# Performance work log

Hardware: AMD Instinct MI355X
Metric: run time of the kernel (lower is better)

## Reference

```python
import jax, jax.numpy as jnp
import numpy as np

HID = 256
HEADS = 8
HD = HID // HEADS  # head_dim = 32


def setup_inputs() -> dict:
    key = jax.random.key(0)
    ks = jax.random.split(key, 16)
    B, N = 4, 2048
    s = 0.02
    inp = {
        'x': jax.random.normal(ks[0], (B, N, 4, HID), dtype=jnp.float32),
        'Wq': jax.random.normal(ks[1], (HID, HID), dtype=jnp.float32) * s,
        'bq': jnp.zeros((HID,), jnp.float32),
        'Wk': jax.random.normal(ks[2], (HID, HID), dtype=jnp.float32) * s,
        'bk': jnp.zeros((HID,), jnp.float32),
        'Wv': jax.random.normal(ks[3], (HID, HID), dtype=jnp.float32) * s,
        'bv': jnp.zeros((HID,), jnp.float32),
        'Wvec': jax.random.normal(ks[4], (2 * HID, HID), dtype=jnp.float32) * s,
        'Wo': jax.random.normal(ks[5], (3 * HID, HID), dtype=jnp.float32) * s,
        'bo': jnp.zeros((3 * HID,), jnp.float32),
        'Wg': jax.random.normal(ks[6], (HID, 2 * HID), dtype=jnp.float32) * s,
        'bg': jnp.zeros((HID,), jnp.float32),
        'alpha_dot': jnp.asarray(1.0, jnp.float32),
        'alpha_norm': jnp.asarray(1.0, jnp.float32),
    }
    return inp


def reference(x, Wq, bq, Wk, bk, Wv, bv, Wvec, Wo, bo, Wg, bg, alpha_dot, alpha_norm):
    B, N, _, H = x.shape
    nh, hd = HEADS, HD
    x_scalar = x[:, :, 0]          # (B,N,H)
    vec = x[:, :, 1:]              # (B,N,3,H)

    def lin(a, W, b=None):
        y = a @ W.T
        return y + b if b is not None else y

    # scalar q/k/v -> (B,heads,N,hd)
    q = lin(x_scalar, Wq, bq).reshape(B, N, nh, hd).transpose(0, 2, 1, 3)
    k = lin(x_scalar, Wk, bk).reshape(B, N, nh, hd).transpose(0, 2, 1, 3)
    v = lin(x_scalar, Wv, bv).reshape(B, N, nh, hd).transpose(0, 2, 1, 3)

    # invariant features from vector channels
    vec_proj = lin(vec, Wvec)                  # (B,N,3,2H)
    vec1, vec2 = vec_proj[..., :H], vec_proj[..., H:]
    vec_dot = jnp.sum(vec1 * vec2, axis=-2)    # (B,N,H)
    vec_norm = jnp.linalg.norm(vec, axis=2)    # (B,N,H)

    # equivariant values: (B,heads,N,3*hd)
    vec_v = vec.reshape(B, N, 3, nh, hd).transpose(0, 3, 1, 2, 4).reshape(B, nh, N, 3 * hd)

    # fused attention: one softmax, aggregate scalar v and vector v together
    scale = 1.0 / np.sqrt(hd).astype(np.float32)
    scores = jnp.einsum('bhqd,bhkd->bhqk', q, k) * scale
    attn = jax.nn.softmax(scores, axis=-1)
    v_all = jnp.concatenate([v, vec_v], axis=-1)        # (B,h,N,4*hd)
    out_all = jnp.einsum('bhqk,bhkd->bhqd', attn, v_all)
    out_s, out_v = out_all[..., :hd], out_all[..., hd:]

    x_out = out_s.transpose(0, 2, 1, 3).reshape(B, N, H)
    vec_aggr = out_v.reshape(B, nh, N, 3, hd).transpose(0, 2, 3, 1, 4).reshape(B, N, 3, H)

    invariants = jnp.concatenate([alpha_dot * vec_dot, alpha_norm * vec_norm], axis=-1)
    gate = jax.nn.sigmoid(lin(invariants, Wg, bg))[:, :, None, :]  # (B,N,1,H)
    vec_combined = gate * vec_aggr + vec  # vector_mixing='add', gating=True

    o = lin(x_out, Wo, bo)
    o1, o2, o3 = o[..., :H], o[..., H:2 * H], o[..., 2 * H:]
    x_updated = vec_dot * o1 + vec_norm * o2 + o3

    x_final = jnp.concatenate([x_updated[:, :, None, :], vec_combined], axis=2)  # (B,N,4,H)
    return x_final
```

## Files before the change

### kernel.cpp

```cpp
#include <hip/hip_runtime.h>
#include <cstdint>
#include <cstddef>

#define HIDN 256
#define NHEAD 8
#define HD 32
#define NSEQ 2048
#define QS (0.17677669529663687f * 1.4426950408889634f)

typedef __attribute__((ext_vector_type(8))) short short8;
typedef __attribute__((ext_vector_type(4))) short short4v;
typedef __attribute__((ext_vector_type(4))) float f32x4;
typedef __attribute__((ext_vector_type(16))) float f32x16;
typedef __attribute__((ext_vector_type(4))) uint32_t u32x4;

static __device__ __forceinline__ short f2bf(float f) {
    union { float f; uint32_t u; } v; v.f = f;
    uint32_t r = (v.u + 0x7FFF + ((v.u >> 16) & 1)) >> 16;
    return (short)r;
}
static __device__ __forceinline__ float bf2f(short s) {
    union { uint32_t u; float f; } v; v.u = ((uint32_t)(uint16_t)s) << 16;
    return v.f;
}

static __device__ __forceinline__ float ex2(float x) {
#if defined(__has_builtin)
#if __has_builtin(__builtin_amdgcn_exp2f)
    return __builtin_amdgcn_exp2f(x);
#else
    return exp2f(x);
#endif
#else
    return exp2f(x);
#endif
}

static __device__ __forceinline__ uint32_t pkbf16(float lo, float hi) {
    uint32_t r;
    asm("v_cvt_pk_bf16_f32 %0, %1, %2" : "=v"(r) : "v"(lo), "v"(hi));
    return r;
}

static __device__ __forceinline__ void half_bcast(uint32_t x, uint32_t& lo, uint32_t& hi) {
    uint32_t a = x, b = x;
    asm("v_permlane32_swap_b32 %0, %1" : "+v"(a), "+v"(b));
    lo = a; hi = b;
}

static __device__ __forceinline__ void gload16(const void* g, void* l) {
    __builtin_amdgcn_global_load_lds(
        (__attribute__((address_space(1))) void*)g,
        (__attribute__((address_space(3))) void*)l, 16, 0, 0);
}

static __device__ __forceinline__ f32x16 zero16() {
    f32x16 z;
    #pragma unroll
    for (int i = 0; i < 16; i++) z[i] = 0.f;
    return z;
}

__global__ __launch_bounds__(256) void wcvt_kernel(
    const float* __restrict__ Wq, const float* __restrict__ Wk,
    const float* __restrict__ Wv, const float* __restrict__ Wvec,
    const float* __restrict__ Wo, const float* __restrict__ Wg,
    const float* __restrict__ bq, const float* __restrict__ bk,
    const float* __restrict__ bv,
    const float* __restrict__ ad, const float* __restrict__ an,
    short* __restrict__ Wqkvb, short* __restrict__ Wvecb,
    short* __restrict__ Wob, short* __restrict__ Wgb, float* __restrict__ bqkvs)
{
    int idx = blockIdx.x * 256 + threadIdx.x;
    if (idx < 65536)        Wqkvb[idx] = f2bf(Wq[idx] * QS);
    else if (idx < 131072)  Wqkvb[idx] = f2bf(Wk[idx - 65536]);
    else if (idx < 196608)  Wqkvb[idx] = f2bf(Wv[idx - 131072]);
    else if (idx < 327680)  Wvecb[idx - 196608] = f2bf(Wvec[idx - 196608]);
    else if (idx < 524288)  Wob[idx - 327680] = f2bf(Wo[idx - 327680]);
    else {
        int i2 = idx - 524288;
        int k = i2 & 511;
        float s = (k < 256) ? ad[0] : an[0];
        Wgb[i2] = f2bf(Wg[i2] * s);
    }
    if (idx < 256)          bqkvs[idx] = bq[idx] * QS;
    else if (idx < 512)     bqkvs[idx] = bk[idx - 256];
    else if (idx < 768)     bqkvs[idx] = bv[idx - 512];
}

__global__ __launch_bounds__(256) void qkv_kernel(
    const float* __restrict__ x, const short* __restrict__ Wqkvb,
    const float* __restrict__ bqkvs,
    short* __restrict__ qbf, short* __restrict__ kbf, short* __restrict__ vtb)
{
    __shared__ short xs[32 * 264];
    __shared__ short vtmp[256 * 34];
    const int tid = threadIdx.x;
    const int m0 = blockIdx.x * 32;
    const int b  = m0 >> 11;
    const int n0 = m0 & 2047;

    #pragma unroll
    for (int l = 0; l < 8; l++) {
        int i = l * 256 + tid;
        int t = i >> 6, j4 = i & 63;
        float4 v = *(const float4*)(x + (size_t)(m0 + t) * 1024 + j4 * 4);
        short4v s = { f2bf(v.x), f2bf(v.y), f2bf(v.z), f2bf(v.w) };
        *(short4v*)&xs[t * 264 + j4 * 4] = s;
    }
    __syncthreads();

    const int wave = tid >> 6, lane = tid & 63;
    const int col = lane & 15, quad = lane >> 4;

    short8 xf[2][8];
    #pragma unroll
    for (int mt = 0; mt < 2; mt++)
        #pragma unroll
        for (int kk = 0; kk < 8; kk++)
            xf[mt][kk] = *(const short8*)&xs[(mt * 16 + col) * 264 + kk * 32 + quad * 8];

    #pragma unroll
    for (int y = 0; y < 3; y++) {
        f32x4 acc[2][4];
        #pragma unroll
        for (int mt = 0; mt < 2; mt++)
            #pragma unroll
            for (int nt = 0; nt < 4; nt++) acc[mt][nt] = (f32x4){0.f,0.f,0.f,0.f};

        const short* Wb = Wqkvb + (size_t)(y * 256 + wave * 64) * 256;
        #pragma unroll
        for (int kk = 0; kk < 8; kk++) {
            #pragma unroll
            for (int nt = 0; nt < 4; nt++) {
                short8 wf = *(const short8*)(Wb + (size_t)(nt * 16 + col) * 256 + kk * 32 + quad * 8);
                #pragma unroll
                for (int mt = 0; mt < 2; mt++)
                    acc[mt][nt] = __builtin_amdgcn_mfma_f32_16x16x32_bf16(wf, xf[mt][kk], acc[mt][nt], 0, 0, 0);
            }
        }

        if (y == 0) {
            #pragma unroll
            for (int nt = 0; nt < 4; nt++) {
                int ch = wave * 64 + nt * 16 + quad * 4;
                float4 bi = *(const float4*)&bqkvs[ch];
                int h = ch >> 5, d = ch & 31;
                #pragma unroll
                for (int mt = 0; mt < 2; mt++) {
                    int n = n0 + mt * 16 + col;
                    short4v s = { f2bf(acc[mt][nt][0] + bi.x), f2bf(acc[mt][nt][1] + bi.y),
                                  f2bf(acc[mt][nt][2] + bi.z), f2bf(acc[mt][nt][3] + bi.w) };
                    *(short4v*)(qbf + ((size_t)(b * 8 + h) * 2048 + n) * 32 + d) = s;
                }
            }
        } else if (y == 1) {
            #pragma unroll
            for (int nt = 0; nt < 4; nt++) {
                int ch = wave * 64 + nt * 16 + quad * 4;
                float4 bi = *(const float4*)&bqkvs[256 + ch];
                int h = ch >> 5, d = ch & 31;
                #pragma unroll
                for (int mt = 0; mt < 2; mt++) {
                    int n = n0 + mt * 16 + col;
                    short4v s = { f2bf(acc[mt][nt][0] + bi.x), f2bf(acc[mt][nt][1] + bi.y),
                                  f2bf(acc[mt][nt][2] + bi.z), f2bf(acc[mt][nt][3] + bi.w) };
                    int f  = ((n & 63) >> 5) * 2 + (d >> 4);
                    int lk = (n & 31) + (((d >> 3) & 1) << 5);
                    short* dst = kbf + ((size_t)(b * 8 + h) * 32 + (n >> 6)) * 2048
                               + f * 512 + lk * 8 + (d & 7);
                    *(short4v*)dst = s;
                }
            }
        } else {
            #pragma unroll
            for (int nt = 0; nt < 4; nt++) {
                int ch = wave * 64 + nt * 16 + quad * 4;
                float4 bi = *(const float4*)&bqkvs[512 + ch];
                #pragma unroll
                for (int mt = 0; mt < 2; mt++) {
                    int tok = mt * 16 + col;
                    vtmp[(ch + 0) * 34 + tok] = f2bf(acc[mt][nt][0] + bi.x);
                    vtmp[(ch + 1) * 34 + tok] = f2bf(acc[mt][nt][1] + bi.y);
                    vtmp[(ch + 2) * 34 + tok] = f2bf(acc[mt][nt][2] + bi.z);
                    vtmp[(ch + 3) * 34 + tok] = f2bf(acc[mt][nt][3] + bi.w);
                }
            }
        }
    }
    __syncthreads();
    {
        int ch = tid;
        short s[32];
        #pragma unroll
        for (int t = 0; t < 32; t++) s[t] = vtmp[ch * 34 + t];
        int h = ch >> 5, d = ch & 31;
        size_t tile = (size_t)(b * 8 + h) * 32 + (n0 >> 6);
        short* dst = vtb + tile * 8192;
        #pragma unroll
        for (int g = 0; g < 4; g++) {
            int kbse = (n0 & 63) + g * 8;
            int f = kbse >> 4;
            int h2 = (kbse >> 3) & 1;
            *(short8*)(dst + f * 512 + (d + h2 * 32) * 8) = *(short8*)&s[g * 8];
        }
    }
}

__global__ __launch_bounds__(512) void vec_kernel(
    const float* __restrict__ x, const short* __restrict__ Wvecb,
    float* __restrict__ dotb, short* __restrict__ invb,
    float* __restrict__ normb, short* __restrict__ vtb)
{
    __shared__ short vb[3 * 16 * 264];
    const int tid = threadIdx.x;
    const int m0 = blockIdx.x * 16;
    const int b = m0 >> 11, n0 = m0 & 2047;

    #pragma unroll
    for (int p = 0; p < 6; p++) {
        int f4 = p * 512 + tid;
        int t = f4 / 192;
        int rem = f4 - t * 192;
        int c = rem >> 6, j4 = rem & 63;
        float4 v = *(const float4*)(x + (size_t)(m0 + t) * 1024 + 256 + c * 256 + j4 * 4);
        short4v s = { f2bf(v.x), f2bf(v.y), f2bf(v.z), f2bf(v.w) };
        *(short4v*)&vb[(c * 16 + t) * 264 + j4 * 4] = s;
    }
    __syncthreads();

    const int wave = tid >> 6, lane = tid & 63;
    const int col = lane & 15, quad = lane >> 4;
    const int j0 = wave * 32;

    f32x4 d1[3][2], d2[3][2];
    #pragma unroll
    for (int c = 0; c < 3; c++)
        #pragma unroll
        for (int nt = 0; nt < 2; nt++) {
            d1[c][nt] = (f32x4){0.f,0.f,0.f,0.f};
            d2[c][nt] = (f32x4){0.f,0.f,0.f,0.f};
        }

    #pragma unroll
    for (int kk = 0; kk < 8; kk++) {
        short8 w1[2], w2[2];
        #pragma unroll
        for (int nt = 0; nt < 2; nt++) {
            w1[nt] = *(const short8*)&Wvecb[(size_t)(j0 + nt * 16 + col) * 256 + kk * 32 + quad * 8];
            w2[nt] = *(const short8*)&Wvecb[(size_t)(256 + j0 + nt * 16 + col) * 256 + kk * 32 + quad * 8];
        }
        #pragma unroll
        for (int c = 0; c < 3; c++) {
            short8 xf = *(const short8*)&vb[(c * 16 + col) * 264 + kk * 32 + quad * 8];
            #pragma unroll
            for (int nt = 0; nt < 2; nt++) {
                d1[c][nt] = __builtin_amdgcn_mfma_f32_16x16x32_bf16(w1[nt], xf, d1[c][nt], 0, 0, 0);
                d2[c][nt] = __builtin_amdgcn_mfma_f32_16x16x32_bf16(w2[nt], xf, d2[c][nt], 0, 0, 0);
            }
        }
    }
    #pragma unroll
    for (int nt = 0; nt < 2; nt++) {
        f32x4 dac = d1[0][nt] * d2[0][nt] + d1[1][nt] * d2[1][nt] + d1[2][nt] * d2[2][nt];
        float4 o = { dac[0], dac[1], dac[2], dac[3] };
        *(float4*)&dotb[(size_t)(m0 + col) * 256 + j0 + nt * 16 + quad * 4] = o;
        short4v s = { f2bf(dac[0]), f2bf(dac[1]), f2bf(dac[2]), f2bf(dac[3]) };
        *(short4v*)&invb[(size_t)(m0 + col) * 512 + j0 + nt * 16 + quad * 4] = s;
    }

    const int j = tid & 255, tp = tid >> 8;
    const int h = j >> 5, d = j & 31;
    #pragma unroll
    for (int t8 = 0; t8 < 8; t8++) {
        int t = tp * 8 + t8;
        float v0 = bf2f(vb[(0 * 16 + t) * 264 + j]);
        float v1 = bf2f(vb[(1 * 16 + t) * 264 + j]);
        float v2 = bf2f(vb[(2 * 16 + t) * 264 + j]);
        float nm = sqrtf(v0 * v0 + v1 * v1 + v2 * v2);
        normb[(size_t)(m0 + t) * 256 + j] = nm;
        invb[(size_t)(m0 + t) * 512 + 256 + j] = f2bf(nm);
    }
    {
        size_t tile = (size_t)(b * 8 + h) * 32 + (n0 >> 6);
        int kbse = (n0 & 63) + tp * 8;
        int ks = kbse >> 4, h2 = (kbse >> 3) & 1;
        #pragma unroll
        for (int c = 0; c < 3; c++) {
            short8 s;
            #pragma unroll
            for (int t8 = 0; t8 < 8; t8++) s[t8] = vb[(c * 16 + tp * 8 + t8) * 264 + j];
            int f = (1 + c) * 4 + ks;
            *(short8*)(vtb + tile * 8192 + f * 512 + (d + h2 * 32) * 8) = s;
        }
    }
}

__global__ __launch_bounds__(256) void attn_kernel(
    const short* __restrict__ qb, const short* __restrict__ kb,
    const short* __restrict__ vtb,
    short* __restrict__ xob, short* __restrict__ ovb)
{
    __shared__ short Ks[2][2048];
    __shared__ short Vs[2][8192];
    const int tid = threadIdx.x;
    const int wave = tid >> 6, lane = tid & 63;
    const int q32 = lane & 31, hi = lane >> 5;

    const int D = blockIdx.x;
    const int slot = D >> 3;
    const int bh = (D & 7) + ((slot & 3) << 3);
    const int qt = slot >> 2;
    const int m0 = qt * 128 + wave * 32;
    const int b = bh >> 3, h = bh & 7;

    const short* qbase = qb + (size_t)bh * NSEQ * HD;
    const short* ksrc  = kb + (size_t)bh * 32 * 2048;
    const short* vsrc  = vtb + (size_t)bh * 32 * 8192;

    short8 qfrag[2];
    #pragma unroll
    for (int ks = 0; ks < 2; ks++)
        qfrag[ks] = *(const short8*)(qbase + (size_t)(m0 + q32) * 32 + ks * 16 + hi * 8);

    f32x16 o[4];
    #pragma unroll
    for (int dt = 0; dt < 4; dt++) o[dt] = zero16();
    float lrun = 0.f;

    auto STAGE = [&](int buf, int t) {
        gload16(ksrc + (size_t)t * 2048 + tid * 8, &Ks[buf][wave * 512]);
        const short* vp = vsrc + (size_t)t * 8192 + tid * 8;
        #pragma unroll
        for (int p = 0; p < 4; p++)
            gload16(vp + p * 2048, &Vs[buf][p * 2048 + wave * 512]);
    };

    STAGE(0, 0);
    __syncthreads();

    for (int kt = 0; kt < 32; kt++) {
        const int cur = kt & 1;
        if (kt < 31) STAGE(cur ^ 1, kt + 1);

        short8 kf[4];
        #pragma unroll
        for (int f = 0; f < 4; f++)
            kf[f] = *(const short8*)&Ks[cur][f * 512 + lane * 8];

        #pragma unroll
        for (int t = 0; t < 2; t++) {
            f32x16 a = zero16();
            a = __builtin_amdgcn_mfma_f32_32x32x16_bf16(kf[2*t+0], qfrag[0], a, 0, 0, 0);
            a = __builtin_amdgcn_mfma_f32_32x32x16_bf16(kf[2*t+1], qfrag[1], a, 0, 0, 0);

            #pragma unroll
            for (int sx = 0; sx < 2; sx++) {
                float e0 = ex2(a[8*sx+0]), e1 = ex2(a[8*sx+1]);
                float e2 = ex2(a[8*sx+2]), e3 = ex2(a[8*sx+3]);
                float e4 = ex2(a[8*sx+4]), e5 = ex2(a[8*sx+5]);
                float e6 = ex2(a[8*sx+6]), e7 = ex2(a[8*sx+7]);
                lrun += ((e0 + e1) + (e2 + e3)) + ((e4 + e5) + (e6 + e7));
                uint32_t al0, ah0, bl0, bh0, al1, ah1, bl1, bh1;
                half_bcast(pkbf16(e0, e1), al0, ah0);
                half_bcast(pkbf16(e2, e3), bl0, bh0);
                half_bcast(pkbf16(e4, e5), al1, ah1);
                half_bcast(pkbf16(e6, e7), bl1, bh1);
                uint32_t u0 = hi ? al1 : al0;
                uint32_t u1 = hi ? bl1 : bl0;
                uint32_t u2 = hi ? ah1 : ah0;
                uint32_t u3 = hi ? bh1 : bh0;
                u32x4 pv = { u0, u1, u2, u3 };
                short8 pf = __builtin_bit_cast(short8, pv);
                const int s = t * 2 + sx;
                #pragma unroll
                for (int dt = 0; dt < 4; dt++) {
                    short8 vf = *(const short8*)&Vs[cur][(dt * 4 + s) * 512 + lane * 8];
                    o[dt] = __builtin_amdgcn_mfma_f32_32x32x16_bf16(vf, pf, o[dt], 0, 0, 0);
                }
            }
        }
        __syncthreads();
    }

    float l = lrun + __shfl_xor(lrun, 32);
    float linv = 1.0f / l;

    size_t mg = (size_t)b * 2048 + m0 + q32;
    short* xr = xob + mg * 256 + h * 32;
    #pragma unroll
    for (int g = 0; g < 4; g++) {
        short4v sv = { f2bf(o[0][4*g+0] * linv), f2bf(o[0][4*g+1] * linv),
                       f2bf(o[0][4*g+2] * linv), f2bf(o[0][4*g+3] * linv) };
        *(short4v*)(xr + g * 8 + hi * 4) = sv;
    }
    short* vr = ovb + mg * 768 + h * 32;
    #pragma unroll
    for (int dt = 1; dt < 4; dt++) {
        #pragma unroll
        for (int g = 0; g < 4; g++) {
            short4v sv = { f2bf(o[dt][4*g+0] * linv), f2bf(o[dt][4*g+1] * linv),
                           f2bf(o[dt][4*g+2] * linv), f2bf(o[dt][4*g+3] * linv) };
            *(short4v*)(vr + (dt - 1) * 256 + g * 8 + hi * 4) = sv;
        }
    }
}

__global__ __launch_bounds__(512, 4) void ogemm_kernel(
    const float* __restrict__ x, const short* __restrict__ xob,
    const short* __restrict__ invb,
    const float* __restrict__ dotb, const float* __restrict__ normb,
    const short* __restrict__ ovb,
    const short* __restrict__ Wob, const short* __restrict__ Wgb,
    const float* __restrict__ bo, const float* __restrict__ bg,
    float* __restrict__ out)
{
    __shared__ __align__(16) union {
        struct { short inv[16 * 520]; short xo[16 * 264]; } in;
        struct { short gate[16 * 264]; short o[16 * 776]; } ob;
    } u;
    const int tid = threadIdx.x;
    const int M0 = blockIdx.x * 16;

    #pragma unroll
    for (int l = 0; l < 2; l++) {
        int i = l * 512 + tid;
        int m = i >> 6, seg = i & 63;
        *(short8*)&u.in.inv[m * 520 + seg * 8] =
            *(const short8*)(invb + (size_t)(M0 + m) * 512 + seg * 8);
    }
    {
        int m = tid >> 5, seg = tid & 31;
        *(short8*)&u.in.xo[m * 264 + seg * 8] =
            *(const short8*)(xob + (size_t)(M0 + m) * 256 + seg * 8);
    }
    __syncthreads();

    const int wave = tid >> 6, lane = tid & 63;
    const int col = lane & 15, quad = lane >> 4;
    const int cg = wave * 32;
    const int co = wave * 96;

    f32x4 accg[2], acco[6];
    #pragma unroll
    for (int i = 0; i < 2; i++) accg[i] = (f32x4){0.f,0.f,0.f,0.f};
    #pragma unroll
    for (int i = 0; i < 6; i++) acco[i] = (f32x4){0.f,0.f,0.f,0.f};

    #pragma unroll
    for (int kk = 0; kk < 8; kk++) {
        short8 wg0 = *(const short8*)(Wgb + (size_t)(cg + col) * 512 + (2*kk) * 32 + quad * 8);
        short8 wg1 = *(const short8*)(Wgb + (size_t)(cg + 16 + col) * 512 + (2*kk) * 32 + quad * 8);
        short8 wg2 = *(const short8*)(Wgb + (size_t)(cg + col) * 512 + (2*kk+1) * 32 + quad * 8);
        short8 wg3 = *(const short8*)(Wgb + (size_t)(cg + 16 + col) * 512 + (2*kk+1) * 32 + quad * 8);
        short8 wo0 = *(const short8*)(Wob + (size_t)(co + 0*16 + col) * 256 + kk * 32 + quad * 8);
        short8 wo1 = *(const short8*)(Wob + (size_t)(co + 1*16 + col) * 256 + kk * 32 + quad * 8);
        short8 wo2 = *(const short8*)(Wob + (size_t)(co + 2*16 + col) * 256 + kk * 32 + quad * 8);
        short8 wo3 = *(const short8*)(Wob + (size_t)(co + 3*16 + col) * 256 + kk * 32 + quad * 8);
        short8 wo4 = *(const short8*)(Wob + (size_t)(co + 4*16 + col) * 256 + kk * 32 + quad * 8);
        short8 wo5 = *(const short8*)(Wob + (size_t)(co + 5*16 + col) * 256 + kk * 32 + quad * 8);
        short8 xg0 = *(const short8*)&u.in.inv[col * 520 + (2*kk) * 32 + quad * 8];
        short8 xg1 = *(const short8*)&u.in.inv[col * 520 + (2*kk+1) * 32 + quad * 8];
        short8 xoo = *(const short8*)&u.in.xo[col * 264 + kk * 32 + quad * 8];
        __builtin_amdgcn_sched_barrier(0);
        accg[0] = __builtin_amdgcn_mfma_f32_16x16x32_bf16(wg0, xg0, accg[0], 0, 0, 0);
        accg[1] = __builtin_amdgcn_mfma_f32_16x16x32_bf16(wg1, xg0, accg[1], 0, 0, 0);
        accg[0] = __builtin_amdgcn_mfma_f32_16x16x32_bf16(wg2, xg1, accg[0], 0, 0, 0);
        accg[1] = __builtin_amdgcn_mfma_f32_16x16x32_bf16(wg3, xg1, accg[1], 0, 0, 0);
        acco[0] = __builtin_amdgcn_mfma_f32_16x16x32_bf16(wo0, xoo, acco[0], 0, 0, 0);
        acco[1] = __builtin_amdgcn_mfma_f32_16x16x32_bf16(wo1, xoo, acco[1], 0, 0, 0);
        acco[2] = __builtin_amdgcn_mfma_f32_16x16x32_bf16(wo2, xoo, acco[2], 0, 0, 0);
        acco[3] = __builtin_amdgcn_mfma_f32_16x16x32_bf16(wo3, xoo, acco[3], 0, 0, 0);
        acco[4] = __builtin_amdgcn_mfma_f32_16x16x32_bf16(wo4, xoo, acco[4], 0, 0, 0);
        acco[5] = __builtin_amdgcn_mfma_f32_16x16x32_bf16(wo5, xoo, acco[5], 0, 0, 0);
    }
    __syncthreads();

    #pragma unroll
    for (int i = 0; i < 2; i++) {
        int ch = cg + i * 16 + quad * 4;
        float4 bi = *(const float4*)&bg[ch];
        short4v s = { f2bf(1.f / (1.f + __expf(-(accg[i][0] + bi.x)))),
                      f2bf(1.f / (1.f + __expf(-(accg[i][1] + bi.y)))),
                      f2bf(1.f / (1.f + __expf(-(accg[i][2] + bi.z)))),
                      f2bf(1.f / (1.f + __expf(-(accg[i][3] + bi.w)))) };
        *(short4v*)&u.ob.gate[col * 264 + ch] = s;
    }
    #pragma unroll
    for (int i = 0; i < 6; i++) {
        int ch = co + i * 16 + quad * 4;
        float4 bi = *(const float4*)&bo[ch];
        short4v s = { f2bf(acco[i][0] + bi.x), f2bf(acco[i][1] + bi.y),
                      f2bf(acco[i][2] + bi.z), f2bf(acco[i][3] + bi.w) };
        *(short4v*)&u.ob.o[col * 776 + ch] = s;
    }
    __syncthreads();

    #pragma unroll
    for (int l = 0; l < 8; l++) {
        int idx4 = l * 512 + tid;
        int m = idx4 >> 8;
        int j = (idx4 & 255) * 4;
        size_t mg = (size_t)(M0 + m);
        if (j < 256) {
            float4 dv = *(const float4*)(dotb + mg * 256 + j);
            float4 nv = *(const float4*)(normb + mg * 256 + j);
            short4v o1 = *(short4v*)&u.ob.o[m * 776 + j];
            short4v o2 = *(short4v*)&u.ob.o[m * 776 + 256 + j];
            short4v o3 = *(short4v*)&u.ob.o[m * 776 + 512 + j];
            float4 r;
            r.x = dv.x * bf2f(o1[0]) + nv.x * bf2f(o2[0]) + bf2f(o3[0]);
            r.y = dv.y * bf2f(o1[1]) + nv.y * bf2f(o2[1]) + bf2f(o3[1]);
            r.z = dv.z * bf2f(o1[2]) + nv.z * bf2f(o2[2]) + bf2f(o3[2]);
            r.w = dv.w * bf2f(o1[3]) + nv.w * bf2f(o2[3]) + bf2f(o3[3]);
            *(float4*)(out + mg * 1024 + j) = r;
        } else {
            int c = (j >> 8) - 1, jj = j & 255;
            short4v g4 = *(short4v*)&u.ob.gate[m * 264 + jj];
            short4v av4 = *(const short4v*)(ovb + mg * 768 + c * 256 + jj);
            float4 xv = *(const float4*)(x + mg * 1024 + 256 + c * 256 + jj);
            float4 r = { bf2f(g4[0]) * bf2f(av4[0]) + xv.x, bf2f(g4[1]) * bf2f(av4[1]) + xv.y,
                         bf2f(g4[2]) * bf2f(av4[2]) + xv.z, bf2f(g4[3]) * bf2f(av4[3]) + xv.w };
            *(float4*)(out + mg * 1024 + j) = r;
        }
    }
}

extern "C" void kernel_launch(void* const* d_in, const int* in_sizes, int n_in,
                              void* d_out, int out_size, void* d_ws, size_t ws_size,
                              hipStream_t stream)
{
    const float* x    = (const float*)d_in[0];
    const float* Wq   = (const float*)d_in[1];
    const float* bq   = (const float*)d_in[2];
    const float* Wk   = (const float*)d_in[3];
    const float* bk   = (const float*)d_in[4];
    const float* Wv   = (const float*)d_in[5];
    const float* bv   = (const float*)d_in[6];
    const float* Wvec = (const float*)d_in[7];
    const float* Wo   = (const float*)d_in[8];
    const float* bo   = (const float*)d_in[9];
    const float* Wg   = (const float*)d_in[10];
    const float* bg   = (const float*)d_in[11];
    const float* adp  = (const float*)d_in[12];
    const float* anp  = (const float*)d_in[13];
    float* out = (float*)d_out;

    float* ws    = (float*)d_ws;
    short* qbf   = (short*)ws;
    short* kbf   = (short*)(ws + 1048576);
    short* vtb   = (short*)(ws + 2097152);
    float* dotb  = ws + 6291456;
    float* normb = ws + 8388608;
    short* xob   = (short*)(ws + 10485760);
    short* ovb   = (short*)(ws + 11534336);
    short* invb  = (short*)(ws + 17825792);
    short* Wqkvb = (short*)(ws + 19922944);
    float* bqkvs = ws + 20021248;
    short* Wvecb = (short*)(ws + 20022016);
    short* Wob   = (short*)(ws + 20087552);
    short* Wgb   = (short*)(ws + 20185856);

    wcvt_kernel<<<2560, 256, 0, stream>>>(Wq, Wk, Wv, Wvec, Wo, Wg, bq, bk, bv,
                                          adp, anp, Wqkvb, Wvecb, Wob, Wgb, bqkvs);
    qkv_kernel<<<256, 256, 0, stream>>>(x, Wqkvb, bqkvs, qbf, kbf, vtb);
    vec_kernel<<<512, 512, 0, stream>>>(x, Wvecb, dotb, invb, normb, vtb);
    attn_kernel<<<512, 256, 0, stream>>>(qbf, kbf, vtb, xob, ovb);
    ogemm_kernel<<<512, 512, 0, stream>>>(x, xob, invb, dotb, normb, ovb,
                                          Wob, Wgb, bo, bg, out);
}
```

Before: 254.9 us.

## Split attention KV loop across two wave groups with LDS reduction

Attention blocks now run 8 waves: two groups of four each process half of the key/value tiles for the same query rows. Group 1 writes its unnormalized output accumulators and row sums into shared memory reusing the staging buffers, and group 0 adds them before normalizing and storing. This halves the serial loop length per wave and raises waves per CU, aiming to hide latency in a low-occupancy kernel. It costs double the shared memory per block and an extra sync plus reduction pass.

After: 253.5 us. About the same (-0.5%).

```diff
diff --git a/kernel.cpp b/kernel.cpp
--- a/kernel.cpp
+++ b/kernel.cpp
@@ -296,22 +296,26 @@
     }
 }
 
-__global__ __launch_bounds__(256) void attn_kernel(
+__global__ __launch_bounds__(512) void attn_kernel(
     const short* __restrict__ qb, const short* __restrict__ kb,
     const short* __restrict__ vtb,
     short* __restrict__ xob, short* __restrict__ ovb)
 {
-    __shared__ short Ks[2][2048];
-    __shared__ short Vs[2][8192];
+    __shared__ __align__(16) union {
+        struct { short Ks[2][2][2048]; short Vs[2][2][8192]; } s;
+        struct { float om[4][16][64][4]; float lm[256]; } m;
+    } u;
     const int tid = threadIdx.x;
     const int wave = tid >> 6, lane = tid & 63;
+    const int g = wave >> 2;
+    const int lwave = wave & 3, lt = tid & 255;
     const int q32 = lane & 31, hi = lane >> 5;
 
     const int D = blockIdx.x;
     const int slot = D >> 3;
     const int bh = (D & 7) + ((slot & 3) << 3);
     const int qt = slot >> 2;
-    const int m0 = qt * 128 + wave * 32;
+    const int m0 = qt * 128 + lwave * 32;
     const int b = bh >> 3, h = bh & 7;
 
     const short* qbase = qb + (size_t)bh * NSEQ * HD;
@@ -329,30 +333,30 @@
     float lrun = 0.f;
 
     auto STAGE = [&](int buf, int t) {
-        gload16(ksrc + (size_t)t * 2048 + tid * 8, &Ks[buf][wave * 512]);
-        const short* vp = vsrc + (size_t)t * 8192 + tid * 8;
+        gload16(ksrc + (size_t)t * 2048 + lt * 8, &u.s.Ks[g][buf][(lt >> 6) * 512]);
+        const short* vp = vsrc + (size_t)t * 8192 + lt * 8;
         #pragma unroll
         for (int p = 0; p < 4; p++)
-            gload16(vp + p * 2048, &Vs[buf][p * 2048 + wave * 512]);
+            gload16(vp + p * 2048, &u.s.Vs[g][buf][p * 2048 + (lt >> 6) * 512]);
     };
 
-    STAGE(0, 0);
-    __syncthreads();
-
-    for (int kt = 0; kt < 32; kt++) {
-        const int cur = kt & 1;
-        if (kt < 31) STAGE(cur ^ 1, kt + 1);
+    STAGE(0, g * 16);
+    __syncthreads();
+
+    for (int t = 0; t < 16; t++) {
+        const int cur = t & 1;
+        if (t < 15) STAGE(cur ^ 1, g * 16 + t + 1);
 
         short8 kf[4];
         #pragma unroll
         for (int f = 0; f < 4; f++)
-            kf[f] = *(const short8*)&Ks[cur][f * 512 + lane * 8];
-
-        #pragma unroll
-        for (int t = 0; t < 2; t++) {
+            kf[f] = *(const short8*)&u.s.Ks[g][cur][f * 512 + lane * 8];
+
+        #pragma unroll
+        for (int tt = 0; tt < 2; tt++) {
             f32x16 a = zero16();
-            a = __builtin_amdgcn_mfma_f32_32x32x16_bf16(kf[2*t+0], qfrag[0], a, 0, 0, 0);
-            a = __builtin_amdgcn_mfma_f32_32x32x16_bf16(kf[2*t+1], qfrag[1], a, 0, 0, 0);
+            a = __builtin_amdgcn_mfma_f32_32x32x16_bf16(kf[2*tt+0], qfrag[0], a, 0, 0, 0);
+            a = __builtin_amdgcn_mfma_f32_32x32x16_bf16(kf[2*tt+1], qfrag[1], a, 0, 0, 0);
 
             #pragma unroll
             for (int sx = 0; sx < 2; sx++) {
@@ -372,10 +376,10 @@
                 uint32_t u3 = hi ? bh1 : bh0;
                 u32x4 pv = { u0, u1, u2, u3 };
                 short8 pf = __builtin_bit_cast(short8, pv);
-                const int s = t * 2 + sx;
+                const int s = tt * 2 + sx;
                 #pragma unroll
                 for (int dt = 0; dt < 4; dt++) {
-                    short8 vf = *(const short8*)&Vs[cur][(dt * 4 + s) * 512 + lane * 8];
+                    short8 vf = *(const short8*)&u.s.Vs[g][cur][(dt * 4 + s) * 512 + lane * 8];
                     o[dt] = __builtin_amdgcn_mfma_f32_32x32x16_bf16(vf, pf, o[dt], 0, 0, 0);
                 }
             }
@@ -383,25 +387,48 @@
         __syncthreads();
     }
 
-    float l = lrun + __shfl_xor(lrun, 32);
-    float linv = 1.0f / l;
-
-    size_t mg = (size_t)b * 2048 + m0 + q32;
-    short* xr = xob + mg * 256 + h * 32;
-    #pragma unroll
-    for (int g = 0; g < 4; g++) {
-        short4v sv = { f2bf(o[0][4*g+0] * linv), f2bf(o[0][4*g+1] * linv),
-                       f2bf(o[0][4*g+2] * linv), f2bf(o[0][4*g+3] * linv) };
-        *(short4v*)(xr + g * 8 + hi * 4) = sv;
-    }
-    short* vr = ovb + mg * 768 + h * 32;
-    #pragma unroll
-    for (int dt = 1; dt < 4; dt++) {
-        #pragma unroll
-        for (int g = 0; g < 4; g++) {
-            short4v sv = { f2bf(o[dt][4*g+0] * linv), f2bf(o[dt][4*g+1] * linv),
-                           f2bf(o[dt][4*g+2] * linv), f2bf(o[dt][4*g+3] * linv) };
-            *(short4v*)(vr + (dt - 1) * 256 + g * 8 + hi * 4) = sv;
+    float lpart = lrun + __shfl_xor(lrun, 32);
+
+    if (g == 1) {
+        #pragma unroll
+        for (int dt = 0; dt < 4; dt++)
+            #pragma unroll
+            for (int q4 = 0; q4 < 4; q4++) {
+                f32x4 c = { o[dt][q4*4+0], o[dt][q4*4+1], o[dt][q4*4+2], o[dt][q4*4+3] };
+                *(f32x4*)&u.m.om[lwave][dt * 4 + q4][lane][0] = c;
+            }
+        u.m.lm[lwave * 64 + lane] = lpart;
+    }
+    __syncthreads();
+    if (g == 0) {
+        #pragma unroll
+        for (int dt = 0; dt < 4; dt++)
+            #pragma unroll
+            for (int q4 = 0; q4 < 4; q4++) {
+                f32x4 c = *(const f32x4*)&u.m.om[lwave][dt * 4 + q4][lane][0];
+                o[dt][q4*4+0] += c[0]; o[dt][q4*4+1] += c[1];
+                o[dt][q4*4+2] += c[2]; o[dt][q4*4+3] += c[3];
+            }
+        float l = lpart + u.m.lm[lwave * 64 + lane];
+        float linv = 1.0f / l;
+
+        size_t mg = (size_t)b * 2048 + m0 + q32;
+        short* xr = xob + mg * 256 + h * 32;
+        #pragma unroll
+        for (int gg = 0; gg < 4; gg++) {
+            short4v sv = { f2bf(o[0][4*gg+0] * linv), f2bf(o[0][4*gg+1] * linv),
+                           f2bf(o[0][4*gg+2] * linv), f2bf(o[0][4*gg+3] * linv) };
+            *(short4v*)(xr + gg * 8 + hi * 4) = sv;
+        }
+        short* vr = ovb + mg * 768 + h * 32;
+        #pragma unroll
+        for (int dt = 1; dt < 4; dt++) {
+            #pragma unroll
+            for (int gg = 0; gg < 4; gg++) {
+                short4v sv = { f2bf(o[dt][4*gg+0] * linv), f2bf(o[dt][4*gg+1] * linv),
+                               f2bf(o[dt][4*gg+2] * linv), f2bf(o[dt][4*gg+3] * linv) };
+                *(short4v*)(vr + (dt - 1) * 256 + gg * 8 + hi * 4) = sv;
+            }
         }
     }
 }
@@ -565,7 +592,7 @@
                                           adp, anp, Wqkvb, Wvecb, Wob, Wgb, bqkvs);
     qkv_kernel<<<256, 256, 0, stream>>>(x, Wqkvb, bqkvs, qbf, kbf, vtb);
     vec_kernel<<<512, 512, 0, stream>>>(x, Wvecb, dotb, invb, normb, vtb);
-    attn_kernel<<<512, 256, 0, stream>>>(qbf, kbf, vtb, xob, ovb);
+    attn_kernel<<<512, 512, 0, stream>>>(qbf, kbf, vtb, xob, ovb);
     ogemm_kernel<<<512, 512, 0, stream>>>(x, xob, invb, dotb, normb, ovb,
                                           Wob, Wgb, bo, bg, out);
 }
```
